# Performance work log

Measured on AMD Instinct MI355X. Metric: run time of the kernel, lower is better.

## Reference

```python
import jax, jax.numpy as jnp
import numpy as np
import math
from jax.scipy.special import gammaln, xlogy

B, N, DIM1, DIM2 = 2, 2048, 1024, 512
H, DK, DV, NRPF = 8, 64, 64, 192


def _pos_embed(seq_len, feat):
    """Enformer-style positional basis: [2*seq_len-1, feat]."""
    nb = feat // 6
    dist = jnp.arange(-seq_len + 1, seq_len, dtype=jnp.float32)
    ad = jnp.abs(dist)[:, None]
    # exponential decay features
    half_life = 2.0 ** jnp.linspace(3.0, math.log2(seq_len), nb)
    f_exp = jnp.exp(-math.log(2.0) / half_life[None, :] * ad)
    # central mask features
    cw = 2.0 ** jnp.arange(1, nb + 1, dtype=jnp.float32) - 1.0
    f_cm = (cw[None, :] > ad).astype(jnp.float32)
    # gamma pdf features
    stddev = seq_len / (2.0 * nb)
    mean = jnp.linspace(seq_len / nb, float(seq_len), nb)[None, :]
    conc = (mean / stddev) ** 2
    rate = mean / stddev ** 2
    log_unnorm = xlogy(conc - 1.0, ad) - rate * ad
    log_norm = gammaln(conc) - conc * jnp.log(rate)
    prob = jnp.exp(log_unnorm - log_norm) + 1e-8
    f_g = prob / jnp.max(prob, axis=-1, keepdims=True)
    emb = jnp.concatenate([f_exp, f_cm, f_g], axis=-1)
    return jnp.concatenate([emb, jnp.sign(dist)[:, None] * emb], axis=-1)


def _relative_shift(x):
    # x: [b, h, t1, t2] with t2 = 2*n - 1 -> [b, h, t1, n]
    b, h, t1, t2 = x.shape
    x = jnp.pad(x, ((0, 0), (0, 0), (0, 0), (1, 0)))
    x = x.reshape(b, h, t2 + 1, t1)[:, :, 1:, :].reshape(b, h, t1, t2)
    return x[..., : (t2 + 2) // 2]


def _forward(x1, x2, Wq, Wk, Wv1, Wv2, Wrel, rel_pos_bias, Wo1, bo1, Wo2, bo2):
    Bb, n1, _ = x1.shape
    n2 = x2.shape[1]
    scale = DK ** -0.5
    split = lambda t, n: t.reshape(Bb, n, H, -1).transpose(0, 2, 1, 3)
    q = split(x1 @ Wq, n1) * scale          # [B,H,n1,DK]
    k = split(x2 @ Wk, n2)                  # [B,H,n2,DK]
    v2 = split(x2 @ Wv2, n2)                # [B,H,n2,DV]
    content = jnp.einsum('bhid,bhjd->bhij', q, k)
    pos = _pos_embed(n1, NRPF)              # [2n1-1, NRPF]
    rel_q = (pos @ Wrel).reshape(-1, H, DK).transpose(1, 0, 2)  # [H,2n1-1,DK]
    rel = jnp.einsum('bhjd,hnd->bhjn', k * scale + rel_pos_bias, rel_q)
    rel = _relative_shift(rel)              # [B,H,n2,n1]
    logits = content + rel.transpose(0, 1, 3, 2)
    attn = jax.nn.softmax(logits, axis=-1)  # [B,H,n1,n2]
    out1 = jnp.einsum('bhij,bhjd->bhid', attn, v2)
    out1 = out1.transpose(0, 2, 1, 3).reshape(Bb, n1, H * DV)
    # exchange=True path: reuse attn transposed with V from x1
    v1 = split(x1 @ Wv1, n1)                # [B,H,n1,DV]
    out2 = jnp.einsum('bhji,bhjd->bhid', attn, v1)
    out2 = out2.transpose(0, 2, 1, 3).reshape(Bb, n2, H * DV)
    return out1 @ Wo1 + bo1, out2 @ Wo2 + bo2


def setup_inputs() -> dict:
    key = jax.random.key(0)
    ks = jax.random.split(key, 10)
    s = lambda fan_in: 1.0 / math.sqrt(fan_in)
    return {
        'x1': jax.random.normal(ks[0], (B, N, DIM1), jnp.float32),
        'x2': jax.random.normal(ks[1], (B, N, DIM2), jnp.float32),
        'Wq': jax.random.normal(ks[2], (DIM1, H * DK), jnp.float32) * s(DIM1),
        'Wk': jax.random.normal(ks[3], (DIM2, H * DK), jnp.float32) * s(DIM2),
        'Wv1': jax.random.normal(ks[4], (DIM1, H * DV), jnp.float32) * s(DIM1),
        'Wv2': jax.random.normal(ks[5], (DIM2, H * DV), jnp.float32) * s(DIM2),
        'Wrel': jax.random.normal(ks[6], (NRPF, H * DK), jnp.float32) * s(NRPF),
        'rel_pos_bias': jax.random.normal(ks[7], (1, H, 1, DK), jnp.float32),
        'Wo1': jax.random.normal(ks[8], (H * DV, DIM1), jnp.float32) * s(H * DV),
        'bo1': jnp.zeros((DIM1,), jnp.float32),
        'Wo2': jax.random.normal(ks[9], (H * DV, DIM1), jnp.float32) * s(H * DV),
        'bo2': jnp.zeros((DIM1,), jnp.float32),
    }


def reference(x1, x2, Wq, Wk, Wv1, Wv2, Wrel, rel_pos_bias, Wo1, bo1, Wo2, bo2):
    return _forward(x1, x2, Wq, Wk, Wv1, Wv2, Wrel, rel_pos_bias, Wo1, bo1, Wo2, bo2)
```

## Files before the change

### kernel.cpp

```cpp
#include <hip/hip_runtime.h>
#include <math.h>

#define NSEQ 2048
#define NPOS 4095
#define NH   8
#define LOG2E 1.4426950408889634f

typedef _Float16 f16;
typedef f16 f16x8 __attribute__((ext_vector_type(8)));
typedef f16 f16x4 __attribute__((ext_vector_type(4)));
typedef float f32x4 __attribute__((ext_vector_type(4)));

#define MFMA16(a,b,c) __builtin_amdgcn_mfma_f32_16x16x32_f16(a,b,c,0,0,0)
#define LSWZ(row, col) (((row) << 7) + ((((col) << 1)) ^ (((row) & 7) << 4)))

__device__ __forceinline__ f16x8 cvt8(float4 a, float4 b) {
  f16x8 r = {(f16)a.x, (f16)a.y, (f16)a.z, (f16)a.w,
             (f16)b.x, (f16)b.y, (f16)b.z, (f16)b.w};
  return r;
}
__device__ __forceinline__ f16x8 scale8(f16x8 v, float4 a, float4 b) {
  f16x8 r;
  r[0] = (f16)((float)v[0] * a.x); r[1] = (f16)((float)v[1] * a.y);
  r[2] = (f16)((float)v[2] * a.z); r[3] = (f16)((float)v[3] * a.w);
  r[4] = (f16)((float)v[4] * b.x); r[5] = (f16)((float)v[5] * b.y);
  r[6] = (f16)((float)v[6] * b.z); r[7] = (f16)((float)v[7] * b.w);
  return r;
}

__global__ __launch_bounds__(256) void pos_embed_k(float* __restrict__ pos) {
  int t = blockIdx.x * 8 + (threadIdx.x >> 5);
  int f = threadIdx.x & 31;
  if (t >= NPOS) return;
  float dist = (float)(t - (NSEQ - 1));
  float ad = fabsf(dist);
  float sgn = (dist > 0.f) ? 1.f : ((dist < 0.f) ? -1.f : 0.f);
  double mean = 64.0 * (double)(f + 1);
  double conc = (mean / 32.0) * (mean / 32.0);
  double rate = mean / 1024.0;
  double p = 0.0;
  if (ad > 0.f) {
    double lu = (conc - 1.0) * log((double)ad) - rate * (double)ad;
    double ln = lgamma(conc) - conc * log(rate);
    p = exp(lu - ln);
  }
  float pf = (float)p + 1e-8f;
  float gmax = pf;
  #pragma unroll
  for (int mk = 1; mk <= 16; mk <<= 1) gmax = fmaxf(gmax, __shfl_xor(gmax, mk));
  float fg = pf / gmax;
  float hl = exp2f(3.f + 8.f * (float)f * (1.f / 31.f));
  float fe = exp2f(-ad / hl);
  float cw = exp2f((float)(f + 1)) - 1.f;
  float fc = (cw > ad) ? 1.f : 0.f;
  float* row = pos + (size_t)t * 192;
  row[f]       = fe;       row[32 + f]  = fc;       row[64 + f]  = fg;
  row[96 + f]  = sgn * fe; row[128 + f] = sgn * fc; row[160 + f] = sgn * fg;
}

__global__ __launch_bounds__(256) void relq_k(
    const float* __restrict__ A, const float* __restrict__ W, f16* __restrict__ relq)
{
  __shared__ f16 As[64][56];
  __shared__ f16 Bs[64][56];
  int tid = threadIdx.x, w = tid >> 6, lane = tid & 63, lr = lane >> 4, lc = lane & 15;
  int m0 = blockIdx.y * 64, n0 = blockIdx.x * 64;
  int ar = tid >> 2, ac = (tid & 3) * 8;
  int bk = tid >> 3, bn = (tid & 7) * 8;
  f32x4 acc[4] = {};
  for (int k0 = 0; k0 < 192; k0 += 32) {
    float4 a0 = make_float4(0.f,0.f,0.f,0.f), a1 = a0;
    if (m0 + ar < NPOS) {
      const float* ap = &A[(size_t)(m0 + ar) * 192 + k0 + ac];
      a0 = *(const float4*)ap; a1 = *(const float4*)(ap + 4);
    }
    *(f16x8*)&As[ar][ac] = cvt8(a0, a1);
    const float* bp = &W[(size_t)(k0 + bk) * 512 + n0 + bn];
    float4 b0 = *(const float4*)bp, b1 = *(const float4*)(bp + 4);
    f16 bv[8] = {(f16)b0.x,(f16)b0.y,(f16)b0.z,(f16)b0.w,(f16)b1.x,(f16)b1.y,(f16)b1.z,(f16)b1.w};
    #pragma unroll
    for (int tt = 0; tt < 8; tt++) { int t = (tt + bk) & 7; Bs[bn + t][bk] = bv[t]; }
    __syncthreads();
    f16x8 af = *(const f16x8*)&As[16*w + lc][8*lr];
    #pragma unroll
    for (int nt = 0; nt < 4; nt++) {
      f16x8 bf = *(const f16x8*)&Bs[16*nt + lc][8*lr];
      acc[nt] = MFMA16(af, bf, acc[nt]);
    }
    __syncthreads();
  }
  #pragma unroll
  for (int nt = 0; nt < 4; nt++)
    #pragma unroll
    for (int r = 0; r < 4; r++) {
      int m = m0 + 16*w + 4*lr + r;
      if (m >= NPOS) continue;
      int nn = n0 + 16*nt + lc;
      relq[((size_t)(nn >> 6) * NPOS + m) * 64 + (nn & 63)] = (f16)(acc[nt][r] * LOG2E);
    }
}

template<int KD, bool SC1>
__global__ __launch_bounds__(256) void projx_k(
    const float* __restrict__ A, const float* __restrict__ W1, const float* __restrict__ W2,
    f16* __restrict__ O1, f16* __restrict__ O2t, const float* __restrict__ rpb)
{
  __shared__ f16 As[64][56];
  __shared__ f16 Bs[64][56];
  int tid = threadIdx.x, w = tid >> 6, lane = tid & 63, lr = lane >> 4, lc = lane & 15;
  int m0 = blockIdx.y * 64, n0g = blockIdx.x * 64;
  bool first = (n0g < 512);
  const float* W = first ? W1 : W2;
  int n0 = n0g & 511;
  int ar = tid >> 2, ac = (tid & 3) * 8;
  int bk = tid >> 3, bn = (tid & 7) * 8;
  f32x4 acc[4] = {};
  for (int k0 = 0; k0 < KD; k0 += 32) {
    const float* ap = &A[(size_t)(m0 + ar) * KD + k0 + ac];
    *(f16x8*)&As[ar][ac] = cvt8(*(const float4*)ap, *(const float4*)(ap + 4));
    const float* bp = &W[(size_t)(k0 + bk) * 512 + n0 + bn];
    float4 b0 = *(const float4*)bp, b1 = *(const float4*)(bp + 4);
    f16 bv[8] = {(f16)b0.x,(f16)b0.y,(f16)b0.z,(f16)b0.w,(f16)b1.x,(f16)b1.y,(f16)b1.z,(f16)b1.w};
    #pragma unroll
    for (int tt = 0; tt < 8; tt++) { int t = (tt + bk) & 7; Bs[bn + t][bk] = bv[t]; }
    __syncthreads();
    f16x8 af = *(const f16x8*)&As[16*w + lc][8*lr];
    #pragma unroll
    for (int nt = 0; nt < 4; nt++) {
      f16x8 bf = *(const f16x8*)&Bs[16*nt + lc][8*lr];
      acc[nt] = MFMA16(af, bf, acc[nt]);
    }
    __syncthreads();
  }
  if (first) {
    #pragma unroll
    for (int nt = 0; nt < 4; nt++)
      #pragma unroll
      for (int r = 0; r < 4; r++) {
        int m = m0 + 16*w + 4*lr + r;
        int nn = n0 + 16*nt + lc;
        float vv = acc[nt][r];
        if (SC1) vv = vv * 0.125f + rpb[nn];
        else     vv = vv * LOG2E;
        O1[(((size_t)((m >> 11) * NH + (nn >> 6))) * NSEQ + (m & (NSEQ - 1))) * 64 + (nn & 63)] = (f16)vv;
      }
  } else {
    int mb = m0 + 16*w + 4*lr;
    #pragma unroll
    for (int nt = 0; nt < 4; nt++) {
      int nn = n0 + 16*nt + lc;
      f16x4 pk = {(f16)acc[nt][0], (f16)acc[nt][1], (f16)acc[nt][2], (f16)acc[nt][3]};
      *(f16x4*)&O2t[(((size_t)((mb >> 11) * NH + (nn >> 6))) * 64 + (nn & 63)) * NSEQ + (mb & (NSEQ - 1))] = pk;
    }
  }
}

__global__ __launch_bounds__(256) void outproj_k(
    const f16* __restrict__ o1, const f16* __restrict__ o2,
    const float* __restrict__ Wo1, const float* __restrict__ Wo2,
    const float* __restrict__ bo1, const float* __restrict__ bo2,
    float* __restrict__ out)
{
  __shared__ f16 As[64][56];
  __shared__ f16 Bs[64][56];
  int by = blockIdx.y;
  bool first = (by < 64);
  const f16* A = first ? o1 : o2;
  const float* W = first ? Wo1 : Wo2;
  const float* bias = first ? bo1 : bo2;
  float* O = out + (first ? 0 : (size_t)4096 * 1024);
  int tid = threadIdx.x, w = tid >> 6, lane = tid & 63, lr = lane >> 4, lc = lane & 15;
  int m0 = (by & 63) * 64, n0 = blockIdx.x * 64;
  int ar = tid >> 2, ac = (tid & 3) * 8;
  int bk = tid >> 3, bn = (tid & 7) * 8;
  f32x4 acc[4] = {};
  for (int k0 = 0; k0 < 512; k0 += 32) {
    *(f16x8*)&As[ar][ac] = *(const f16x8*)&A[(size_t)(m0 + ar) * 512 + k0 + ac];
    const float* bp = &W[(size_t)(k0 + bk) * 1024 + n0 + bn];
    float4 b0 = *(const float4*)bp, b1 = *(const float4*)(bp + 4);
    f16 bv[8] = {(f16)b0.x,(f16)b0.y,(f16)b0.z,(f16)b0.w,(f16)b1.x,(f16)b1.y,(f16)b1.z,(f16)b1.w};
    #pragma unroll
    for (int tt = 0; tt < 8; tt++) { int t = (tt + bk) & 7; Bs[bn + t][bk] = bv[t]; }
    __syncthreads();
    f16x8 af = *(const f16x8*)&As[16*w + lc][8*lr];
    #pragma unroll
    for (int nt = 0; nt < 4; nt++) {
      f16x8 bf = *(const f16x8*)&Bs[16*nt + lc][8*lr];
      acc[nt] = MFMA16(af, bf, acc[nt]);
    }
    __syncthreads();
  }
  #pragma unroll
  for (int nt = 0; nt < 4; nt++)
    #pragma unroll
    for (int r = 0; r < 4; r++) {
      int m = m0 + 16*w + 4*lr + r;
      int n = n0 + 16*nt + lc;
      O[(size_t)m * 1024 + n] = acc[nt][r] + bias[n];
    }
}

__global__ __launch_bounds__(256) void attn_k(
    const f16* __restrict__ q, const f16* __restrict__ kb,
    const f16* __restrict__ relq, const f16* __restrict__ v2t,
    f16* __restrict__ attnT, float* __restrict__ fac_t,
    f16* __restrict__ o1acc, int bh0)
{
  __shared__ char smem[40960];
  char* QG = smem;
  char* KB = smem + 8192;
  char* R0 = smem + 16384;
  char* R1 = smem + 24576;
  char* VS = smem + 32768;
  int z = blockIdx.y, bh = bh0 + z, b = bh >> 3, h = bh & 7;
  int i0 = blockIdx.x * 64;
  int tid = threadIdx.x, w = tid >> 6, lane = tid & 63;
  int lr = lane >> 4, lc = lane & 15;
  char* PW = KB + w * 2048;
  int base0 = i0 + 1984;
  int row = tid >> 2, c0 = (tid & 3) * 16;

  {
    const f16* qp = q + ((size_t)bh * NSEQ + i0 + row) * 64 + c0;
    *(f16x8*)(QG + LSWZ(row, c0))     = *(const f16x8*)qp;
    *(f16x8*)(QG + LSWZ(row, c0 + 8)) = *(const f16x8*)(qp + 8);
    const f16* rp = relq + ((size_t)h * NPOS + base0 + 64 + row) * 64 + c0;
    *(f16x8*)(R1 + LSWZ(row, c0))     = *(const f16x8*)rp;
    *(f16x8*)(R1 + LSWZ(row, c0 + 8)) = *(const f16x8*)(rp + 8);
  }
  __syncthreads();
  f16x8 qa0 = *(const f16x8*)(QG + LSWZ(16*w + lc, 8*lr));
  f16x8 qa1 = *(const f16x8*)(QG + LSWZ(16*w + lc, 32 + 8*lr));

  const f16* kpb  = kb  + ((size_t)bh * NSEQ + row) * 64 + c0;
  const f16* vpb  = v2t + ((size_t)bh * 64 + row) * NSEQ + c0;
  const f16* rpb0 = relq + ((size_t)h * NPOS + base0 + row) * 64 + c0;
  f16x8 skb0 = *(const f16x8*)kpb,  skb1 = *(const f16x8*)(kpb + 8);
  f16x8 sv0  = *(const f16x8*)vpb,  sv1  = *(const f16x8*)(vpb + 8);
  f16x8 sr0  = *(const f16x8*)rpb0, sr1  = *(const f16x8*)(rpb0 + 8);

  float m_run[4], ssum[4];
  float mreg0[4] = {}, mreg1[4] = {};
  f32x4 o1a[4] = {};
  #pragma unroll
  for (int r = 0; r < 4; r++) { m_run[r] = -1e30f; ssum[r] = 0.f; }

  for (int jt = 0; jt < 32; jt++) {
    int j0 = jt * 64;
    char* RsA = (jt & 1) ? R1 : R0;
    char* RsB = (jt & 1) ? R0 : R1;
    *(f16x8*)(KB + LSWZ(row, c0))      = skb0;  *(f16x8*)(KB + LSWZ(row, c0 + 8))  = skb1;
    *(f16x8*)(VS + LSWZ(row, c0))      = sv0;   *(f16x8*)(VS + LSWZ(row, c0 + 8))  = sv1;
    *(f16x8*)(RsA + LSWZ(row, c0))     = sr0;   *(f16x8*)(RsA + LSWZ(row, c0 + 8)) = sr1;
    __syncthreads();
    f32x4 cacc[4];
    f16x8 ka0 = {}, ka1 = {};
    __builtin_amdgcn_s_setprio(1);
    #pragma unroll
    for (int y = 0; y < 4; y++) {
      f16x8 b0 = *(const f16x8*)(KB + LSWZ(16*y + lc, 8*lr));
      f16x8 b1 = *(const f16x8*)(KB + LSWZ(16*y + lc, 32 + 8*lr));
      f32x4 t = {};
      t = MFMA16(qa0, b0, t);
      t = MFMA16(qa1, b1, t);
      cacc[y] = t;
      if (y == w) { ka0 = b0; ka1 = b1; }
    }
    __builtin_amdgcn_s_setprio(0);
    #pragma unroll
    for (int gg = 0; gg < 5; gg++) {
      int g = 3 - w + gg;
      char* Rg = (g < 4) ? RsA : RsB;
      int grow = 16 * (g & 3) + lc;
      f32x4 ga = {};
      ga = MFMA16(ka0, *(const f16x8*)(Rg + LSWZ(grow, 8*lr)), ga);
      ga = MFMA16(ka1, *(const f16x8*)(Rg + LSWZ(grow, 32 + 8*lr)), ga);
      int jj = 16*w + 4*lr;
      #pragma unroll
      for (int r = 0; r < 4; r++) {
        int ii = 16*g + lc + jj + r - 63;
        if ((unsigned)ii < 64u) *(f16*)(QG + LSWZ(jj + r, ii)) = (f16)ga[r];
      }
    }
    {
      int jn = (jt < 31) ? jt + 1 : 31;
      const f16* kpn = kb  + ((size_t)bh * NSEQ + jn * 64 + row) * 64 + c0;
      const f16* vpn = v2t + ((size_t)bh * 64 + row) * NSEQ + jn * 64 + c0;
      const f16* rpn = relq + ((size_t)h * NPOS + base0 - 64 * jn + row) * 64 + c0;
      skb0 = *(const f16x8*)kpn;  skb1 = *(const f16x8*)(kpn + 8);
      sv0  = *(const f16x8*)vpn;  sv1  = *(const f16x8*)(vpn + 8);
      sr0  = *(const f16x8*)rpn;  sr1  = *(const f16x8*)(rpn + 8);
    }
    __syncthreads();
    float l[4][4];
    #pragma unroll
    for (int y = 0; y < 4; y++) {
      f16x4 gv = *(const f16x4*)(QG + LSWZ(16*y + lc, 16*w + 4*lr));
      #pragma unroll
      for (int r = 0; r < 4; r++) l[y][r] = cacc[y][r] + (float)gv[r];
    }
    float pvr[4][4];
    #pragma unroll
    for (int r = 0; r < 4; r++) {
      float tm = fmaxf(fmaxf(l[0][r], l[1][r]), fmaxf(l[2][r], l[3][r]));
      #pragma unroll
      for (int mk = 1; mk <= 8; mk <<= 1) tm = fmaxf(tm, __shfl_xor(tm, mk));
      if (tm > m_run[r]) {
        float sc = exp2f(m_run[r] - tm);
        ssum[r] *= sc;
        #pragma unroll
        for (int nt = 0; nt < 4; nt++) o1a[nt][r] *= sc;
        m_run[r] = tm;
      }
      float mnew = m_run[r];
      float ps = 0.f;
      #pragma unroll
      for (int y = 0; y < 4; y++) {
        float p = exp2f(l[y][r] - mnew);
        ps += p;
        pvr[r][y] = p;
        *(f16*)(PW + LSWZ(4*lr + r, 16*y + lc)) = (f16)p;
      }
      ssum[r] += ps;
      if (jt < 16) { if (lc == jt) mreg0[r] = mnew; }
      else         { if (lc == jt - 16) mreg1[r] = mnew; }
    }
    #pragma unroll
    for (int y = 0; y < 4; y++) {
      f16x4 pk = {(f16)pvr[0][y], (f16)pvr[1][y], (f16)pvr[2][y], (f16)pvr[3][y]};
      *(f16x4*)&attnT[((size_t)z * NSEQ + j0 + 16*y + lc) * NSEQ + i0 + 16*w + 4*lr] = pk;
    }
    {
      f16x8 pa0 = *(const f16x8*)(PW + LSWZ(lc, 8*lr));
      f16x8 pa1 = *(const f16x8*)(PW + LSWZ(lc, 32 + 8*lr));
      __builtin_amdgcn_s_setprio(1);
      #pragma unroll
      for (int nt = 0; nt < 4; nt++) {
        f16x8 vf0 = *(const f16x8*)(VS + LSWZ(16*nt + lc, 8*lr));
        f16x8 vf1 = *(const f16x8*)(VS + LSWZ(16*nt + lc, 32 + 8*lr));
        o1a[nt] = MFMA16(pa0, vf0, o1a[nt]);
        o1a[nt] = MFMA16(pa1, vf1, o1a[nt]);
      }
      __builtin_amdgcn_s_setprio(0);
    }
    __syncthreads();
  }
  float invs[4];
  #pragma unroll
  for (int r = 0; r < 4; r++) {
    float s = ssum[r];
    #pragma unroll
    for (int mk = 1; mk <= 8; mk <<= 1) s += __shfl_xor(s, mk);
    invs[r] = 1.f / s;
    int il = 16*w + 4*lr + r;
    float mf = m_run[r];
    #pragma unroll
    for (int jtb = 0; jtb < 2; jtb++) {
      int jt = jtb * 16 + lc;
      float mv = (jtb == 0) ? mreg0[r] : mreg1[r];
      float fv = exp2f(mv - mf) * invs[r];
      fac_t[((size_t)z * 32 + jt) * NSEQ + i0 + il] = fv;
    }
  }
  #pragma unroll
  for (int nt = 0; nt < 4; nt++)
    #pragma unroll
    for (int r = 0; r < 4; r++) {
      int rw = i0 + 16*w + 4*lr + r;
      o1acc[((size_t)b * NSEQ + rw) * 512 + h * 64 + 16*nt + lc] = (f16)(o1a[nt][r] * invs[r]);
    }
}

__global__ __launch_bounds__(256) void pv2_k(const f16* __restrict__ attnT,
    const f16* __restrict__ v1t, const float* __restrict__ fac_t,
    f16* __restrict__ oacc, int bh0)
{
  __shared__ char vsm[8192];
  int z = blockIdx.y, bh = bh0 + z, b = bh >> 3, h = bh & 7;
  int r0 = blockIdx.x * 64;
  int tid = threadIdx.x, w = tid >> 6, lane = tid & 63;
  int lr = lane >> 4, lc = lane & 15;
  int row = tid >> 2, cv = (tid & 3) * 16;
  const f16* vp = v1t + ((size_t)bh * 64 + row) * NSEQ + cv;
  const float* fp = fac_t + ((size_t)z * 32 + blockIdx.x) * NSEQ + cv;
  const f16* ap = attnT + ((size_t)z * NSEQ + r0 + 16*w + lc) * NSEQ + 8*lr;
  f32x4 acc[4] = {};
  for (int k0 = 0; k0 < NSEQ; k0 += 64) {
    f16x8 v0 = *(const f16x8*)(vp + k0);
    f16x8 v1 = *(const f16x8*)(vp + k0 + 8);
    float4 f0 = *(const float4*)(fp + k0),     f1 = *(const float4*)(fp + k0 + 4);
    float4 f2 = *(const float4*)(fp + k0 + 8), f3 = *(const float4*)(fp + k0 + 12);
    *(f16x8*)(vsm + LSWZ(row, cv))     = scale8(v0, f0, f1);
    *(f16x8*)(vsm + LSWZ(row, cv + 8)) = scale8(v1, f2, f3);
    __syncthreads();
    f16x8 a0 = *(const f16x8*)(ap + k0);
    f16x8 a1 = *(const f16x8*)(ap + k0 + 32);
    #pragma unroll
    for (int nt = 0; nt < 4; nt++) {
      acc[nt] = MFMA16(a0, *(const f16x8*)(vsm + LSWZ(16*nt + lc, 8*lr)), acc[nt]);
      acc[nt] = MFMA16(a1, *(const f16x8*)(vsm + LSWZ(16*nt + lc, 32 + 8*lr)), acc[nt]);
    }
    __syncthreads();
  }
  #pragma unroll
  for (int nt = 0; nt < 4; nt++)
    #pragma unroll
    for (int r = 0; r < 4; r++) {
      int rw = r0 + 16*w + 4*lr + r;
      oacc[((size_t)b * NSEQ + rw) * 512 + h * 64 + 16*nt + lc] = (f16)acc[nt][r];
    }
}

extern "C" void kernel_launch(void* const* d_in, const int* in_sizes, int n_in,
                              void* d_out, int out_size, void* d_ws, size_t ws_size,
                              hipStream_t stream) {
  const float* x1   = (const float*)d_in[0];
  const float* x2   = (const float*)d_in[1];
  const float* Wq   = (const float*)d_in[2];
  const float* Wk   = (const float*)d_in[3];
  const float* Wv1  = (const float*)d_in[4];
  const float* Wv2  = (const float*)d_in[5];
  const float* Wrel = (const float*)d_in[6];
  const float* rpb  = (const float*)d_in[7];
  const float* Wo1  = (const float*)d_in[8];
  const float* bo1  = (const float*)d_in[9];
  const float* Wo2  = (const float*)d_in[10];
  const float* bo2  = (const float*)d_in[11];
  float* out = (float*)d_out;

  char* base = (char*)d_ws;
  size_t off = 0;
  auto alloc = [&](size_t bytes) -> void* {
    void* p = base + off; off += (bytes + 255) & ~(size_t)255; return p;
  };
  float* pos   = (float*)alloc((size_t)NPOS * 192 * 4);
  f16*   relq  = (f16*)  alloc((size_t)NH * NPOS * 64 * 2);
  f16*   qh    = (f16*)  alloc((size_t)16 * NSEQ * 64 * 2);
  f16*   kbh   = (f16*)  alloc((size_t)16 * NSEQ * 64 * 2);
  f16*   v1t   = (f16*)  alloc((size_t)16 * 64 * NSEQ * 2);
  f16*   v2t   = (f16*)  alloc((size_t)16 * 64 * NSEQ * 2);
  f16*   o1acc = (f16*)  alloc((size_t)2 * NSEQ * 512 * 2);
  f16*   o2acc = (f16*)  alloc((size_t)2 * NSEQ * 512 * 2);
  float* fac_t = (float*)alloc((size_t)16 * 32 * NSEQ * 4);
  size_t baseB = off;

  int chunk = 1;
  for (int c = 16; c >= 1; c >>= 1) {
    size_t needB = baseB + (size_t)c * NSEQ * NSEQ * 2;
    if (needB <= ws_size) { chunk = c; break; }
  }
  f16* attnT = (f16*)(base + baseB);

  pos_embed_k<<<(NPOS + 7) / 8, 256, 0, stream>>>(pos);
  relq_k<<<dim3(8, 64), 256, 0, stream>>>(pos, Wrel, relq);
  projx_k<1024, false><<<dim3(16, 64), 256, 0, stream>>>(x1, Wq, Wv1, qh, v1t, nullptr);
  projx_k<512,  true ><<<dim3(16, 64), 256, 0, stream>>>(x2, Wk, Wv2, kbh, v2t, rpb);

  for (int bh0 = 0; bh0 < 16; bh0 += chunk) {
    attn_k<<<dim3(32, chunk), 256, 0, stream>>>(qh, kbh, relq, v2t, attnT, fac_t, o1acc, bh0);
    pv2_k<<<dim3(32, chunk), 256, 0, stream>>>(attnT, v1t, fac_t, o2acc, bh0);
  }

  outproj_k<<<dim3(16, 128), 256, 0, stream>>>(o1acc, o2acc, Wo1, Wo2, bo1, bo2, out);
}
```

Before: 302.4 us.

## Split attention key loop across two warp groups with flash-style merge

The attention kernel now launches 512 threads per block. Two 256-thread groups each process half of the key tiles with their own shared buffers, then merge their running max, sum and partial PV outputs through shared memory. The goal is more parallelism per query tile, since the grid has only 32×chunk blocks. The cost is doubled LDS use per block (80KB), which may limit occupancy, plus extra synchronisation and merge work.

```diff
diff --git a/kernel.cpp b/kernel.cpp
--- a/kernel.cpp
+++ b/kernel.cpp
@@ -200,52 +200,59 @@
     }
 }
 
-__global__ __launch_bounds__(256) void attn_k(
+__global__ __launch_bounds__(512) void attn_k(
     const f16* __restrict__ q, const f16* __restrict__ kb,
     const f16* __restrict__ relq, const f16* __restrict__ v2t,
     f16* __restrict__ attnT, float* __restrict__ fac_t,
     f16* __restrict__ o1acc, int bh0)
 {
-  __shared__ char smem[40960];
-  char* QG = smem;
-  char* KB = smem + 8192;
-  char* R0 = smem + 16384;
-  char* R1 = smem + 24576;
-  char* VS = smem + 32768;
+  __shared__ char smem[81920];
+  char* G2A = smem;
   int z = blockIdx.y, bh = bh0 + z, b = bh >> 3, h = bh & 7;
   int i0 = blockIdx.x * 64;
-  int tid = threadIdx.x, w = tid >> 6, lane = tid & 63;
-  int lr = lane >> 4, lc = lane & 15;
-  char* PW = KB + w * 2048;
+  int tid = threadIdx.x;
+  int wg = tid >> 8;
+  int tg = tid & 255;
+  int w4 = (tid >> 6) & 3;
+  int lane = tid & 63, lr = lane >> 4, lc = lane & 15;
+  char* GRP = smem + 16384 + wg * 32768;
+  char* KB = GRP;
+  char* VS = GRP + 8192;
+  char* R0 = GRP + 16384;
+  char* R1 = GRP + 24576;
+  char* G2 = smem + wg * 8192;
+  char* PW = KB + w4 * 2048;
+  int jt0 = wg * 16;
   int base0 = i0 + 1984;
-  int row = tid >> 2, c0 = (tid & 3) * 16;
-
+  int row = tg >> 2, c0 = (tg & 3) * 16;
+
+  if (tid < 256) {
+    const f16* qp = q + ((size_t)bh * NSEQ + i0 + row) * 64 + c0;
+    *(f16x8*)(G2A + LSWZ(row, c0))     = *(const f16x8*)qp;
+    *(f16x8*)(G2A + LSWZ(row, c0 + 8)) = *(const f16x8*)(qp + 8);
+  }
   {
-    const f16* qp = q + ((size_t)bh * NSEQ + i0 + row) * 64 + c0;
-    *(f16x8*)(QG + LSWZ(row, c0))     = *(const f16x8*)qp;
-    *(f16x8*)(QG + LSWZ(row, c0 + 8)) = *(const f16x8*)(qp + 8);
-    const f16* rp = relq + ((size_t)h * NPOS + base0 + 64 + row) * 64 + c0;
+    const f16* rp = relq + ((size_t)h * NPOS + base0 + 64 - 64*jt0 + row) * 64 + c0;
     *(f16x8*)(R1 + LSWZ(row, c0))     = *(const f16x8*)rp;
     *(f16x8*)(R1 + LSWZ(row, c0 + 8)) = *(const f16x8*)(rp + 8);
   }
   __syncthreads();
-  f16x8 qa0 = *(const f16x8*)(QG + LSWZ(16*w + lc, 8*lr));
-  f16x8 qa1 = *(const f16x8*)(QG + LSWZ(16*w + lc, 32 + 8*lr));
-
-  const f16* kpb  = kb  + ((size_t)bh * NSEQ + row) * 64 + c0;
-  const f16* vpb  = v2t + ((size_t)bh * 64 + row) * NSEQ + c0;
-  const f16* rpb0 = relq + ((size_t)h * NPOS + base0 + row) * 64 + c0;
+  f16x8 qa0 = *(const f16x8*)(G2A + LSWZ(16*w4 + lc, 8*lr));
+  f16x8 qa1 = *(const f16x8*)(G2A + LSWZ(16*w4 + lc, 32 + 8*lr));
+
+  const f16* kpb  = kb  + ((size_t)bh * NSEQ + jt0 * 64 + row) * 64 + c0;
+  const f16* vpb  = v2t + ((size_t)bh * 64 + row) * NSEQ + jt0 * 64 + c0;
+  const f16* rpb0 = relq + ((size_t)h * NPOS + base0 - 64*jt0 + row) * 64 + c0;
   f16x8 skb0 = *(const f16x8*)kpb,  skb1 = *(const f16x8*)(kpb + 8);
   f16x8 sv0  = *(const f16x8*)vpb,  sv1  = *(const f16x8*)(vpb + 8);
   f16x8 sr0  = *(const f16x8*)rpb0, sr1  = *(const f16x8*)(rpb0 + 8);
 
-  float m_run[4], ssum[4];
-  float mreg0[4] = {}, mreg1[4] = {};
+  float m_run[4], ssum[4], mreg[4] = {};
   f32x4 o1a[4] = {};
   #pragma unroll
   for (int r = 0; r < 4; r++) { m_run[r] = -1e30f; ssum[r] = 0.f; }
 
-  for (int jt = 0; jt < 32; jt++) {
+  for (int jt = jt0; jt < jt0 + 16; jt++) {
     int j0 = jt * 64;
     char* RsA = (jt & 1) ? R1 : R0;
     char* RsB = (jt & 1) ? R0 : R1;
@@ -264,26 +271,26 @@
       t = MFMA16(qa0, b0, t);
       t = MFMA16(qa1, b1, t);
       cacc[y] = t;
-      if (y == w) { ka0 = b0; ka1 = b1; }
+      if (y == w4) { ka0 = b0; ka1 = b1; }
     }
     __builtin_amdgcn_s_setprio(0);
     #pragma unroll
     for (int gg = 0; gg < 5; gg++) {
-      int g = 3 - w + gg;
+      int g = 3 - w4 + gg;
       char* Rg = (g < 4) ? RsA : RsB;
       int grow = 16 * (g & 3) + lc;
       f32x4 ga = {};
       ga = MFMA16(ka0, *(const f16x8*)(Rg + LSWZ(grow, 8*lr)), ga);
       ga = MFMA16(ka1, *(const f16x8*)(Rg + LSWZ(grow, 32 + 8*lr)), ga);
-      int jj = 16*w + 4*lr;
+      int jj = 16*w4 + 4*lr;
       #pragma unroll
       for (int r = 0; r < 4; r++) {
         int ii = 16*g + lc + jj + r - 63;
-        if ((unsigned)ii < 64u) *(f16*)(QG + LSWZ(jj + r, ii)) = (f16)ga[r];
+        if ((unsigned)ii < 64u) *(f16*)(G2 + LSWZ(jj + r, ii)) = (f16)ga[r];
       }
     }
     {
-      int jn = (jt < 31) ? jt + 1 : 31;
+      int jn = (jt < jt0 + 15) ? jt + 1 : jt;
       const f16* kpn = kb  + ((size_t)bh * NSEQ + jn * 64 + row) * 64 + c0;
       const f16* vpn = v2t + ((size_t)bh * 64 + row) * NSEQ + jn * 64 + c0;
       const f16* rpn = relq + ((size_t)h * NPOS + base0 - 64 * jn + row) * 64 + c0;
@@ -295,7 +302,7 @@
     float l[4][4];
     #pragma unroll
     for (int y = 0; y < 4; y++) {
-      f16x4 gv = *(const f16x4*)(QG + LSWZ(16*y + lc, 16*w + 4*lr));
+      f16x4 gv = *(const f16x4*)(G2 + LSWZ(16*y + lc, 16*w4 + 4*lr));
       #pragma unroll
       for (int r = 0; r < 4; r++) l[y][r] = cacc[y][r] + (float)gv[r];
     }
@@ -322,13 +329,12 @@
         *(f16*)(PW + LSWZ(4*lr + r, 16*y + lc)) = (f16)p;
       }
       ssum[r] += ps;
-      if (jt < 16) { if (lc == jt) mreg0[r] = mnew; }
-      else         { if (lc == jt - 16) mreg1[r] = mnew; }
+      if (lc == jt - jt0) mreg[r] = mnew;
     }
     #pragma unroll
     for (int y = 0; y < 4; y++) {
       f16x4 pk = {(f16)pvr[0][y], (f16)pvr[1][y], (f16)pvr[2][y], (f16)pvr[3][y]};
-      *(f16x4*)&attnT[((size_t)z * NSEQ + j0 + 16*y + lc) * NSEQ + i0 + 16*w + 4*lr] = pk;
+      *(f16x4*)&attnT[((size_t)z * NSEQ + j0 + 16*y + lc) * NSEQ + i0 + 16*w4 + 4*lr] = pk;
     }
     {
       f16x8 pa0 = *(const f16x8*)(PW + LSWZ(lc, 8*lr));
@@ -345,30 +351,49 @@
     }
     __syncthreads();
   }
-  float invs[4];
+  float* stats = (float*)(smem + 65536);
+  float* o1x   = (float*)(smem + 32768);
+  float invs[4], mfin[4];
   #pragma unroll
   for (int r = 0; r < 4; r++) {
     float s = ssum[r];
     #pragma unroll
     for (int mk = 1; mk <= 8; mk <<= 1) s += __shfl_xor(s, mk);
-    invs[r] = 1.f / s;
-    int il = 16*w + 4*lr + r;
-    float mf = m_run[r];
-    #pragma unroll
-    for (int jtb = 0; jtb < 2; jtb++) {
-      int jt = jtb * 16 + lc;
-      float mv = (jtb == 0) ? mreg0[r] : mreg1[r];
-      float fv = exp2f(mv - mf) * invs[r];
-      fac_t[((size_t)z * 32 + jt) * NSEQ + i0 + il] = fv;
-    }
-  }
-  #pragma unroll
-  for (int nt = 0; nt < 4; nt++)
-    #pragma unroll
-    for (int r = 0; r < 4; r++) {
-      int rw = i0 + 16*w + 4*lr + r;
-      o1acc[((size_t)b * NSEQ + rw) * 512 + h * 64 + 16*nt + lc] = (f16)(o1a[nt][r] * invs[r]);
-    }
+    int il = 16*w4 + 4*lr + r;
+    if (lc == 0) { stats[(wg*64 + il)*2] = m_run[r]; stats[(wg*64 + il)*2 + 1] = s; }
+  }
+  __syncthreads();
+  #pragma unroll
+  for (int r = 0; r < 4; r++) {
+    int il = 16*w4 + 4*lr + r;
+    float m0v = stats[il*2],        s0v = stats[il*2 + 1];
+    float m1v = stats[(64+il)*2],   s1v = stats[(64+il)*2 + 1];
+    float mf = fmaxf(m0v, m1v);
+    float sf = s0v * exp2f(m0v - mf) + s1v * exp2f(m1v - mf);
+    mfin[r] = mf; invs[r] = 1.f / sf;
+    float fv = exp2f(mreg[r] - mf) * invs[r];
+    fac_t[((size_t)z * 32 + jt0 + lc) * NSEQ + i0 + il] = fv;
+  }
+  if (wg == 1) {
+    #pragma unroll
+    for (int nt = 0; nt < 4; nt++)
+      #pragma unroll
+      for (int r = 0; r < 4; r++) {
+        int il = 16*w4 + 4*lr + r;
+        o1x[il*64 + 16*nt + lc] = o1a[nt][r] * exp2f(m_run[r] - mfin[r]);
+      }
+  }
+  __syncthreads();
+  if (wg == 0) {
+    #pragma unroll
+    for (int nt = 0; nt < 4; nt++)
+      #pragma unroll
+      for (int r = 0; r < 4; r++) {
+        int il = 16*w4 + 4*lr + r;
+        float val = (o1a[nt][r] * exp2f(m_run[r] - mfin[r]) + o1x[il*64 + 16*nt + lc]) * invs[r];
+        o1acc[((size_t)b * NSEQ + i0 + il) * 512 + h * 64 + 16*nt + lc] = (f16)val;
+      }
+  }
 }
 
 __global__ __launch_bounds__(256) void pv2_k(const f16* __restrict__ attnT,
@@ -457,7 +482,7 @@
   projx_k<512,  true ><<<dim3(16, 64), 256, 0, stream>>>(x2, Wk, Wv2, kbh, v2t, rpb);
 
   for (int bh0 = 0; bh0 < 16; bh0 += chunk) {
-    attn_k<<<dim3(32, chunk), 256, 0, stream>>>(qh, kbh, relq, v2t, attnT, fac_t, o1acc, bh0);
+    attn_k<<<dim3(32, chunk), 512, 0, stream>>>(qh, kbh, relq, v2t, attnT, fac_t, o1acc, bh0);
     pv2_k<<<dim3(32, chunk), 256, 0, stream>>>(attnT, v1t, fac_t, o2acc, bh0);
   }
 
```

After: 319.1 us. +5.5%, slower.
